# Performance work log

Hardware: AMD Instinct MI355X
Metric: run time of the kernel (lower is better)

The kernel has to match this reference:

```python
import jax, jax.numpy as jnp
import numpy as np

N = 100000   # nodes
E = 1600000  # edges (before self-loops)
H = 4        # heads
C = 16       # out channels per head
NEG_SLOPE = 0.2


def _gat_layer(x, src, dst, W, a_src, a_dst, b):
    # x: [N, Fin]; W: [Fin, H*C]; a_src/a_dst: [H, C]; b: [H*C]
    h = (x @ W).reshape(N, H, C)                       # [N, H, C]
    e_s = jnp.einsum('nhc,hc->nh', h, a_src)           # [N, H]
    e_d = jnp.einsum('nhc,hc->nh', h, a_dst)           # [N, H]
    e = e_s[src] + e_d[dst]                            # [E', H]
    e = jax.nn.leaky_relu(e, NEG_SLOPE)
    # segment softmax over destination nodes
    m = jax.ops.segment_max(e, dst, num_segments=N)    # [N, H]
    ex = jnp.exp(e - m[dst])
    s = jax.ops.segment_sum(ex, dst, num_segments=N)   # [N, H]
    alpha = ex / (s[dst] + 1e-16)                      # [E', H]
    msg = alpha[:, :, None] * h[src]                   # [E', H, C]
    out = jax.ops.segment_sum(msg, dst, num_segments=N)  # [N, H, C]
    return out.reshape(N, H * C) + b


def setup_inputs() -> dict:
    key = jax.random.key(0)
    ks = jax.random.split(key, 24)
    g = lambda k, shp, sc=0.1: (jax.random.normal(k, shp, jnp.float32) * sc)
    inp = {
        'x': jax.random.normal(ks[0], (N, 1), jnp.float32),
        'edge_index': jax.random.randint(ks[1], (2, E), 0, N, dtype=jnp.int32),
        # GAT layer 0: in=1
        'W0': g(ks[2], (1, H * C)), 'as0': g(ks[3], (H, C)), 'ad0': g(ks[4], (H, C)), 'b0': jnp.zeros((H * C,), jnp.float32),
        # GAT layer 1: in=64
        'W1': g(ks[5], (H * C, H * C)), 'as1': g(ks[6], (H, C)), 'ad1': g(ks[7], (H, C)), 'b1': jnp.zeros((H * C,), jnp.float32),
        # GAT layer 2: in=64
        'W2': g(ks[8], (H * C, H * C)), 'as2': g(ks[9], (H, C)), 'ad2': g(ks[10], (H, C)), 'b2': jnp.zeros((H * C,), jnp.float32),
        # latent MLP: Linear(64,64) -> ReLU -> Linear(64,16)
        'lw1': g(ks[11], (H * C, 64)), 'lb1': jnp.zeros((64,), jnp.float32),
        'lw2': g(ks[12], (64, 16)), 'lb2': jnp.zeros((16,), jnp.float32),
        # decoder: Linear(16,4) -> Softmax
        'dw': g(ks[13], (16, 4)), 'db': jnp.zeros((4,), jnp.float32),
    }
    return inp


def reference(x, edge_index, W0, as0, ad0, b0, W1, as1, ad1, b1, W2, as2, ad2, b2, lw1, lb1, lw2, lb2, dw, db):
    # add self-loops (PyG GATConv default add_self_loops=True)
    loops = jnp.arange(N, dtype=edge_index.dtype)
    src = jnp.concatenate([edge_index[0], loops])
    dst = jnp.concatenate([edge_index[1], loops])
    h = _gat_layer(x, src, dst, W0, as0, ad0, b0)
    h = _gat_layer(h, src, dst, W1, as1, ad1, b1)
    h = _gat_layer(h, src, dst, W2, as2, ad2, b2)
    h = jax.nn.relu(h @ lw1 + lb1)
    h = h @ lw2 + lb2
    logits = h @ dw + db
    return jax.nn.softmax(logits, axis=-1)
```

## Files before the change

kernel.cpp:

```cpp
#include <hip/hip_runtime.h>
#include <hip/hip_fp16.h>
#include <math.h>

#define NN 100000
#define EE 1600000
#define EP (EE + NN)
#define NEG 0.2f
#define TN 128
#define BW 256
#define NB 391
#define CHUNK 4096
#define SSTRIDE 5120
#define SCAP 5120

typedef __attribute__((ext_vector_type(2))) float floatx2;

__device__ inline unsigned pk_fp8x4(float a, float b, float c, float d) {
    unsigned r = __builtin_amdgcn_cvt_pk_fp8_f32(a, b, 0u, false);
    r = __builtin_amdgcn_cvt_pk_fp8_f32(c, d, r, true);
    return r;
}

__device__ __forceinline__ void accum_fp8p(uint2 raw, float p, floatx2* acc) {
    floatx2 p2; p2[0] = p; p2[1] = p;
    acc[0] += p2 * __builtin_amdgcn_cvt_pk_f32_fp8(raw.x, false);
    acc[1] += p2 * __builtin_amdgcn_cvt_pk_f32_fp8(raw.x, true);
    acc[2] += p2 * __builtin_amdgcn_cvt_pk_f32_fp8(raw.y, false);
    acc[3] += p2 * __builtin_amdgcn_cvt_pk_f32_fp8(raw.y, true);
}

__device__ __forceinline__ int wave_iscan(int v, int lane) {
#pragma unroll
    for (int o = 1; o < 64; o <<= 1) {
        int t = __shfl_up(v, o);
        if (lane >= o) v += t;
    }
    return v;
}


__global__ __launch_bounds__(512) void partition_k(const int* __restrict__ ei, int* __restrict__ gcur,
                                                   unsigned int* __restrict__ arena) {
    __shared__ int lh[512], lcur[512], lbase[512];
    __shared__ int wsum[8];
    __shared__ unsigned int staged[CHUNK];
    __shared__ unsigned short stb[CHUNK];
    int tid = threadIdx.x;
    int lane = tid & 63, wid = tid >> 6;
    int c0 = blockIdx.x * CHUNK;
    int csize = min(CHUNK, EP - c0);
    lh[tid] = 0;
    __syncthreads();
    unsigned int myv[8];
    int myb[8];
#pragma unroll
    for (int i = 0; i < 8; i++) {
        int e = c0 + i * 512 + tid;
        if (e < c0 + csize) {
            int d = (e < EE) ? ei[EE + e] : (e - EE);
            int sv = (e < EE) ? ei[e] : d;
            int b = d >> 8;
            myv[i] = ((unsigned)(d - (b << 8)) << 17) | (unsigned)sv;
            myb[i] = b;
            atomicAdd(&lh[b], 1);
        } else myb[i] = -1;
    }
    __syncthreads();
    int v = lh[tid];
    int isc = wave_iscan(v, lane);
    if (lane == 63) wsum[wid] = isc;
    __syncthreads();
    if (tid == 0) {
        int run = 0;
#pragma unroll
        for (int w = 0; w < 8; w++) { int t = wsum[w]; wsum[w] = run; run += t; }
    }
    __syncthreads();
    int excl = isc - v + wsum[wid];
    lcur[tid] = excl;
    __syncthreads();
#pragma unroll
    for (int i = 0; i < 8; i++) {
        if (myb[i] >= 0) {
            int idx = atomicAdd(&lcur[myb[i]], 1);
            staged[idx] = myv[i];
            stb[idx] = (unsigned short)myb[i];
        }
    }
    __syncthreads();
    if (tid < NB && v > 0) {
        int base = atomicAdd(&gcur[tid], v);
        lbase[tid] = tid * SSTRIDE + base - excl;
    }
    __syncthreads();
    for (int i = tid; i < csize; i += 512) {
        unsigned int val = staged[i];
        arena[lbase[stb[i]] + i] = val;
    }
}

__global__ __launch_bounds__(512) void bscan_k(const int* __restrict__ gcur, int* __restrict__ bbase,
                                               int* __restrict__ rowptr) {
    __shared__ int s[512];
    int tid = threadIdx.x;
    int v = (tid < NB) ? gcur[tid] : 0;
    s[tid] = v;
    __syncthreads();
    for (int o = 1; o < 512; o <<= 1) {
        int t = (tid >= o) ? s[tid - o] : 0;
        __syncthreads();
        s[tid] += t;
        __syncthreads();
    }
    int excl = s[tid] - v;
    if (tid <= NB) bbase[tid] = excl;
    if (tid == 0) rowptr[NN] = EP;
}

__global__ __launch_bounds__(512) void csr_scatter_k(const int* __restrict__ bbase, const int* __restrict__ gcur,
                                                     const unsigned int* __restrict__ arena,
                                                     int* __restrict__ rowptr, int* __restrict__ edge_src) {
    __shared__ int cnt[256], sc[256];
    __shared__ int wsum[4];
    __shared__ unsigned int stg[SCAP];
    int tid = threadIdx.x;
    int b = blockIdx.x;
    int e0 = bbase[b];
    int sz = gcur[b];
    int abase = b * SSTRIDE;
    if (tid < 256) cnt[tid] = 0;
    __syncthreads();
    for (int i = tid; i < sz; i += 512) {
        unsigned int v = arena[abase + i];
        if (i < SCAP) stg[i] = v;
        atomicAdd(&cnt[v >> 17], 1);
    }
    __syncthreads();
    if (tid < 256) {
        int lane = tid & 63, wid = tid >> 6;
        int v = cnt[tid];
        int isc = wave_iscan(v, lane);
        if (lane == 63) wsum[wid] = isc;
        __syncthreads();
        if (tid == 0) {
            int run = 0;
#pragma unroll
            for (int w = 0; w < 4; w++) { int t = wsum[w]; wsum[w] = run; run += t; }
        }
        __syncthreads();
        int excl = isc - v + wsum[wid];
        int d = (b << 8) + tid;
        if (d < NN) rowptr[d] = e0 + excl;
        sc[tid] = excl;
    } else {
        __syncthreads();
        __syncthreads();
    }
    __syncthreads();
    for (int i = tid; i < sz; i += 512) {
        unsigned int val = (i < SCAP) ? stg[i] : arena[abase + i];
        int dl = val >> 17;
        int p = atomicAdd(&sc[dl], 1);
        edge_src[e0 + p] = (int)(val & 0x1FFFFu);
    }
}


__global__ __launch_bounds__(256) void gather0_k(const float* __restrict__ x, const float* __restrict__ W0,
                                                 const float* __restrict__ as_, const float* __restrict__ ad_,
                                                 const int* __restrict__ rowptr, const int* __restrict__ edge_src,
                                                 const float* __restrict__ b, __half* __restrict__ hout) {
    __shared__ float W0l[64], asl[64], adl[64], bl[64];
    int tid = threadIdx.x;
    if (tid < 64) { W0l[tid] = W0[tid]; asl[tid] = as_[tid]; adl[tid] = ad_[tid]; bl[tid] = b[tid]; }
    __syncthreads();
    int wv = (blockIdx.x * 256 + tid) >> 6;
    int lane = tid & 63;
    if (wv >= NN) return;
    int q = lane >> 2, head = lane & 3;
    float cs = 0.f, cd = 0.f;
#pragma unroll
    for (int c = 0; c < 16; c++) {
        float w = W0l[head * 16 + c];
        cs += w * asl[head * 16 + c];
        cd += w * adl[head * 16 + c];
    }
    int beg = rowptr[wv], end = rowptr[wv + 1];
    float xd = x[wv];
    float num = 0.f, den = 0.f;
    for (int e0 = beg; e0 < end; e0 += 16) {
        int e = e0 + q;
        bool vld = e < end;
        int ee = vld ? e : (end - 1);
        int src = edge_src[ee];
        float xs = x[src];
        float ev = xs * cs + xd * cd;
        ev = ev > 0.f ? ev : NEG * ev;
        float p = vld ? __expf(ev) : 0.f;
        num += p * xs;
        den += p;
    }
    num += __shfl_xor(num, 4);  num += __shfl_xor(num, 8);
    num += __shfl_xor(num, 16); num += __shfl_xor(num, 32);
    den += __shfl_xor(den, 4);  den += __shfl_xor(den, 8);
    den += __shfl_xor(den, 16); den += __shfl_xor(den, 32);
    float nh = __shfl(num, lane >> 4);
    float dh = __shfl(den, lane >> 4);
    float val = nh / (dh + 1e-16f);
    float hv = val * W0l[lane] + bl[lane];
    hout[((size_t)wv << 6) + lane] = __float2half(hv);
}


__global__ __launch_bounds__(256) void transform64_k(const __half* __restrict__ hin, const float* __restrict__ W,
                                                     const float* __restrict__ as_, const float* __restrict__ ad_,
                                                     unsigned char* __restrict__ h8, float* __restrict__ es, float* __restrict__ ed) {
    __shared__ float At[64 * TN];
    __shared__ float Wl[64 * 64];
    int tid = threadIdx.x;
    for (int i = tid; i < 4096; i += 256) Wl[i] = W[i];
    int n0 = blockIdx.x * TN;
    {
        int row = tid >> 1, hf = tid & 1;
        int n = n0 + row;
        const uint4* src = (const uint4*)(hin + ((size_t)n << 6) + (hf << 5));
#pragma unroll
        for (int i = 0; i < 4; i++) {
            uint4 raw = make_uint4(0, 0, 0, 0);
            if (n < NN) raw = src[i];
            __half2* hh = (__half2*)&raw;
            int c = (hf << 5) + (i << 3);
#pragma unroll
            for (int j = 0; j < 4; j++) {
                float2 f = __half22float2(hh[j]);
                At[(c + 2 * j) * TN + row]     = f.x;
                At[(c + 2 * j + 1) * TN + row] = f.y;
            }
        }
    }
    __syncthreads();
    int c = tid & 15, r = tid >> 4;
    float acc[8][4];
#pragma unroll
    for (int i = 0; i < 8; i++)
#pragma unroll
        for (int j = 0; j < 4; j++) acc[i][j] = 0.f;
#pragma unroll 4
    for (int k = 0; k < 64; k++) {
        float4 a0 = *(float4*)&At[k * TN + r * 8];
        float4 a1 = *(float4*)&At[k * TN + r * 8 + 4];
        float4 w  = *(float4*)&Wl[k * 64 + c * 4];
        float av[8] = {a0.x, a0.y, a0.z, a0.w, a1.x, a1.y, a1.z, a1.w};
#pragma unroll
        for (int i = 0; i < 8; i++) {
            acc[i][0] += av[i] * w.x; acc[i][1] += av[i] * w.y;
            acc[i][2] += av[i] * w.z; acc[i][3] += av[i] * w.w;
        }
    }
    int head = c >> 2, qq = c & 3;
    float as0v = as_[head * 16 + qq * 4], as1v = as_[head * 16 + qq * 4 + 1];
    float as2v = as_[head * 16 + qq * 4 + 2], as3v = as_[head * 16 + qq * 4 + 3];
    float ad0v = ad_[head * 16 + qq * 4], ad1v = ad_[head * 16 + qq * 4 + 1];
    float ad2v = ad_[head * 16 + qq * 4 + 2], ad3v = ad_[head * 16 + qq * 4 + 3];
#pragma unroll
    for (int i = 0; i < 8; i++) {
        int n = n0 + r * 8 + i;
        float pes = acc[i][0] * as0v + acc[i][1] * as1v + acc[i][2] * as2v + acc[i][3] * as3v;
        float ped = acc[i][0] * ad0v + acc[i][1] * ad1v + acc[i][2] * ad2v + acc[i][3] * ad3v;
        pes += __shfl_xor(pes, 1); pes += __shfl_xor(pes, 2);
        ped += __shfl_xor(ped, 1); ped += __shfl_xor(ped, 2);
        if (n < NN) {
            unsigned rq = pk_fp8x4(acc[i][0], acc[i][1], acc[i][2], acc[i][3]);
            *(unsigned*)(h8 + ((size_t)n << 6) + (c << 2)) = rq;
            if (qq == 0) { es[n * 4 + head] = pes; ed[n * 4 + head] = ped; }
        }
    }
}


__global__ __launch_bounds__(256) void gather_k(const unsigned char* __restrict__ h8, const float* __restrict__ es,
                                                const float* __restrict__ ed, const int* __restrict__ rowptr,
                                                const int* __restrict__ edge_src, const float* __restrict__ b,
                                                __half* __restrict__ hout) {
    int pr = (blockIdx.x * 256 + threadIdx.x) >> 6;
    int lane = threadIdx.x & 63;
    int nA = pr * 2;
    if (nA >= NN) return;
    int nB = nA + 1;
    bool hasB = nB < NN;
    int q = lane >> 3, j = lane & 7, head = j >> 1;
    const unsigned char* h8j = h8 + (j << 3);
    int begA = rowptr[nA], endA = rowptr[nA + 1];
    int begB = hasB ? rowptr[nB] : begA, endB = hasB ? rowptr[nB + 1] : begA;
    float edvA = ed[nA * 4 + head];
    float edvB = hasB ? ed[nB * 4 + head] : 0.f;
    floatx2 accA[4], accB[4];
#pragma unroll
    for (int t = 0; t < 4; t++) { accA[t] = (floatx2)(0.f); accB[t] = (floatx2)(0.f); }
    float sA = 0.f, sB = 0.f;
    int iters = max((endA - begA + 7) >> 3, (endB - begB + 7) >> 3);
    for (int k = 0; k < iters; k++) {
        int eA = begA + (k << 3) + q;
        int eB = begB + (k << 3) + q;
        bool vA = eA < endA;
        bool vB = eB < endB;
        int srcA = edge_src[vA ? eA : begA];
        int srcB = edge_src[vB ? eB : begB];
        uint2 rawA = *(const uint2*)(h8j + ((unsigned)srcA << 6));
        float esvA = es[srcA * 4 + head];
        uint2 rawB = *(const uint2*)(h8j + ((unsigned)srcB << 6));
        float esvB = es[srcB * 4 + head];
        float evA = esvA + edvA; evA = evA > 0.f ? evA : NEG * evA;
        float evB = esvB + edvB; evB = evB > 0.f ? evB : NEG * evB;
        float pA = vA ? __expf(evA) : 0.f;
        float pB = vB ? __expf(evB) : 0.f;
        accum_fp8p(rawA, pA, accA);
        accum_fp8p(rawB, pB, accB);
        sA += pA;
        sB += pB;
    }
    float fA[8], fB[8];
#pragma unroll
    for (int t = 0; t < 4; t++) {
        fA[2 * t] = accA[t][0]; fA[2 * t + 1] = accA[t][1];
        fB[2 * t] = accB[t][0]; fB[2 * t + 1] = accB[t][1];
    }
#pragma unroll
    for (int t = 0; t < 8; t++) {
        fA[t] += __shfl_xor(fA[t], 8);
        fA[t] += __shfl_xor(fA[t], 16);
        fA[t] += __shfl_xor(fA[t], 32);
        fB[t] += __shfl_xor(fB[t], 8);
        fB[t] += __shfl_xor(fB[t], 16);
        fB[t] += __shfl_xor(fB[t], 32);
    }
    sA += __shfl_xor(sA, 8); sA += __shfl_xor(sA, 16); sA += __shfl_xor(sA, 32);
    sB += __shfl_xor(sB, 8); sB += __shfl_xor(sB, 16); sB += __shfl_xor(sB, 32);
    if (q == 0) {
        const float4* bp = (const float4*)(b + j * 8);
        float4 b0 = bp[0], b1 = bp[1];
        {
            float inv = 1.0f / (sA + 1e-16f);
            union { __half2 h2[4]; uint4 u; } pk;
            pk.h2[0] = __floats2half2_rn(fA[0] * inv + b0.x, fA[1] * inv + b0.y);
            pk.h2[1] = __floats2half2_rn(fA[2] * inv + b0.z, fA[3] * inv + b0.w);
            pk.h2[2] = __floats2half2_rn(fA[4] * inv + b1.x, fA[5] * inv + b1.y);
            pk.h2[3] = __floats2half2_rn(fA[6] * inv + b1.z, fA[7] * inv + b1.w);
            *(uint4*)(hout + ((size_t)nA << 6) + (j << 3)) = pk.u;
        }
        if (hasB) {
            float inv = 1.0f / (sB + 1e-16f);
            union { __half2 h2[4]; uint4 u; } pk;
            pk.h2[0] = __floats2half2_rn(fB[0] * inv + b0.x, fB[1] * inv + b0.y);
            pk.h2[1] = __floats2half2_rn(fB[2] * inv + b0.z, fB[3] * inv + b0.w);
            pk.h2[2] = __floats2half2_rn(fB[4] * inv + b1.x, fB[5] * inv + b1.y);
            pk.h2[3] = __floats2half2_rn(fB[6] * inv + b1.z, fB[7] * inv + b1.w);
            *(uint4*)(hout + ((size_t)nB << 6) + (j << 3)) = pk.u;
        }
    }
}


__global__ __launch_bounds__(256) void mlp_k(const __half* __restrict__ h, const float* __restrict__ lw1,
                                             const float* __restrict__ lb1, const float* __restrict__ lw2,
                                             const float* __restrict__ lb2, const float* __restrict__ dw,
                                             const float* __restrict__ db, float* __restrict__ out) {
    __shared__ float At[64 * TN];
    __shared__ float W1l[4096];
    __shared__ float W2l[1024];
    __shared__ float dwl[64];
    __shared__ float dbl[4];
    int tid = threadIdx.x;
    for (int i = tid; i < 4096; i += 256) W1l[i] = lw1[i];
    for (int i = tid; i < 1024; i += 256) W2l[i] = lw2[i];
    if (tid < 64) dwl[tid] = dw[tid];
    if (tid < 4) dbl[tid] = db[tid];
    int n0 = blockIdx.x * TN;
    {
        int row = tid >> 1, hf = tid & 1;
        int n = n0 + row;
        const uint4* src = (const uint4*)(h + ((size_t)n << 6) + (hf << 5));
#pragma unroll
        for (int i = 0; i < 4; i++) {
            uint4 raw = make_uint4(0, 0, 0, 0);
            if (n < NN) raw = src[i];
            __half2* hh = (__half2*)&raw;
            int c = (hf << 5) + (i << 3);
#pragma unroll
            for (int j = 0; j < 4; j++) {
                float2 f = __half22float2(hh[j]);
                At[(c + 2 * j) * TN + row]     = f.x;
                At[(c + 2 * j + 1) * TN + row] = f.y;
            }
        }
    }
    __syncthreads();
    int c = tid & 15, r = tid >> 4;
    float acc[8][4];
#pragma unroll
    for (int i = 0; i < 8; i++)
#pragma unroll
        for (int j = 0; j < 4; j++) acc[i][j] = 0.f;
#pragma unroll 4
    for (int k = 0; k < 64; k++) {
        float4 a0 = *(float4*)&At[k * TN + r * 8];
        float4 a1 = *(float4*)&At[k * TN + r * 8 + 4];
        float4 w  = *(float4*)&W1l[k * 64 + c * 4];
        float av[8] = {a0.x, a0.y, a0.z, a0.w, a1.x, a1.y, a1.z, a1.w};
#pragma unroll
        for (int i = 0; i < 8; i++) {
            acc[i][0] += av[i] * w.x; acc[i][1] += av[i] * w.y;
            acc[i][2] += av[i] * w.z; acc[i][3] += av[i] * w.w;
        }
    }
    float b1v0 = lb1[c * 4], b1v1 = lb1[c * 4 + 1], b1v2 = lb1[c * 4 + 2], b1v3 = lb1[c * 4 + 3];
    __syncthreads();
#pragma unroll
    for (int i = 0; i < 8; i++) {
        int n = r * 8 + i;
        At[(c * 4 + 0) * TN + n] = fmaxf(acc[i][0] + b1v0, 0.f);
        At[(c * 4 + 1) * TN + n] = fmaxf(acc[i][1] + b1v1, 0.f);
        At[(c * 4 + 2) * TN + n] = fmaxf(acc[i][2] + b1v2, 0.f);
        At[(c * 4 + 3) * TN + n] = fmaxf(acc[i][3] + b1v3, 0.f);
    }
    __syncthreads();
    float acc2[8];
#pragma unroll
    for (int i = 0; i < 8; i++) acc2[i] = 0.f;
#pragma unroll 4
    for (int k = 0; k < 64; k++) {
        float4 a0 = *(float4*)&At[k * TN + r * 8];
        float4 a1 = *(float4*)&At[k * TN + r * 8 + 4];
        float wv = W2l[k * 16 + c];
        acc2[0] += a0.x * wv; acc2[1] += a0.y * wv; acc2[2] += a0.z * wv; acc2[3] += a0.w * wv;
        acc2[4] += a1.x * wv; acc2[5] += a1.y * wv; acc2[6] += a1.z * wv; acc2[7] += a1.w * wv;
    }
    float b2v = lb2[c];
#pragma unroll
    for (int i = 0; i < 8; i++) W1l[c * TN + r * 8 + i] = acc2[i] + b2v;
    __syncthreads();
    if (tid < TN) {
        int n = n0 + tid;
        if (n < NN) {
            float lg0 = dbl[0], lg1 = dbl[1], lg2 = dbl[2], lg3 = dbl[3];
#pragma unroll
            for (int k = 0; k < 16; k++) {
                float a = W1l[k * TN + tid];
                lg0 += a * dwl[k * 4];     lg1 += a * dwl[k * 4 + 1];
                lg2 += a * dwl[k * 4 + 2]; lg3 += a * dwl[k * 4 + 3];
            }
            float mx = fmaxf(fmaxf(lg0, lg1), fmaxf(lg2, lg3));
            float e0 = __expf(lg0 - mx), e1 = __expf(lg1 - mx), e2 = __expf(lg2 - mx), e3 = __expf(lg3 - mx);
            float inv = 1.0f / (e0 + e1 + e2 + e3);
            *(float4*)(out + (size_t)n * 4) = make_float4(e0 * inv, e1 * inv, e2 * inv, e3 * inv);
        }
    }
}


extern "C" void kernel_launch(void* const* d_in, const int* in_sizes, int n_in,
                              void* d_out, int out_size, void* d_ws, size_t ws_size,
                              hipStream_t stream) {
    const float* x   = (const float*)d_in[0];
    const int*   ei  = (const int*)d_in[1];
    const float* W0  = (const float*)d_in[2];
    const float* as0 = (const float*)d_in[3];
    const float* ad0 = (const float*)d_in[4];
    const float* b0  = (const float*)d_in[5];
    const float* W1  = (const float*)d_in[6];
    const float* as1 = (const float*)d_in[7];
    const float* ad1 = (const float*)d_in[8];
    const float* b1  = (const float*)d_in[9];
    const float* W2  = (const float*)d_in[10];
    const float* as2 = (const float*)d_in[11];
    const float* ad2 = (const float*)d_in[12];
    const float* b2  = (const float*)d_in[13];
    const float* lw1 = (const float*)d_in[14];
    const float* lb1 = (const float*)d_in[15];
    const float* lw2 = (const float*)d_in[16];
    const float* lb2 = (const float*)d_in[17];
    const float* dw  = (const float*)d_in[18];
    const float* db  = (const float*)d_in[19];
    float* out = (float*)d_out;

    char* p = (char*)d_ws;
    size_t off = 0;
    auto alloc = [&](size_t n) -> void* {
        void* r = p + off;
        off = (off + n + 255) & ~(size_t)255;
        return r;
    };
    __half* hB     = (__half*)alloc((size_t)NN * 64 * 2);
    __half* hC     = (__half*)alloc((size_t)NN * 64 * 2);
    unsigned char* h8 = (unsigned char*)alloc((size_t)NN * 64);
    float*  es     = (float*)alloc((size_t)NN * 4 * 4);
    float*  ed     = (float*)alloc((size_t)NN * 4 * 4);
    int*    rowptr = (int*)alloc((size_t)(NN + 1) * 4);
    int*    edge_src = (int*)alloc((size_t)EP * 4);
    unsigned int* arena = (unsigned int*)alloc((size_t)NB * SSTRIDE * 4);
    int*    gcur   = (int*)alloc(512 * 4);
    int*    bbase  = (int*)alloc(513 * 4);

    hipMemsetAsync(gcur, 0, 512 * 4, stream);

    partition_k<<<(EP + CHUNK - 1) / CHUNK, 512, 0, stream>>>(ei, gcur, arena);
    bscan_k<<<1, 512, 0, stream>>>(gcur, bbase, rowptr);
    csr_scatter_k<<<NB, 512, 0, stream>>>(bbase, gcur, arena, rowptr, edge_src);

    int nb_tile = (NN + TN - 1) / TN;
    int nb_wave = (NN + 3) / 4;
    int nb_pair = ((NN + 1) / 2 + 3) / 4;

    gather0_k<<<nb_wave, 256, 0, stream>>>(x, W0, as0, ad0, rowptr, edge_src, b0, hB);

    transform64_k<<<nb_tile, 256, 0, stream>>>(hB, W1, as1, ad1, h8, es, ed);
    gather_k<<<nb_pair, 256, 0, stream>>>(h8, es, ed, rowptr, edge_src, b1, hC);

    transform64_k<<<nb_tile, 256, 0, stream>>>(hC, W2, as2, ad2, h8, es, ed);
    gather_k<<<nb_pair, 256, 0, stream>>>(h8, es, ed, rowptr, edge_src, b2, hB);

    mlp_k<<<nb_tile, 256, 0, stream>>>(hB, lw1, lb1, lw2, lb2, dw, db, out);
}
```

Baseline: 311.2 us.

## Fuse each GAT gather with the next transform or MLP through LDS tiles

Merges the per-layer gather kernel with the following 64x64 transform (and the last gather with the MLP/decoder) so each 128-node tile's aggregated features stay in swizzled fp16 LDS instead of going through global fp16 buffers. This cuts the launch count from six to three and removes the global write and read of the intermediate fp16 node features. Intermediate buffers are double-buffered (h8a/h8b, es/ed pairs) so a fused kernel can read the previous layer's output while writing its own. In exchange, each 512-thread block does the gather serially per wave (16 nodes per wave) before the GEMM, which could lower latency hiding and occupancy because of the larger LDS footprint.

```diff
diff --git a/kernel.cpp b/kernel.cpp
--- a/kernel.cpp
+++ b/kernel.cpp
@@ -7,7 +7,6 @@
 #define EP (EE + NN)
 #define NEG 0.2f
 #define TN 128
-#define BW 256
 #define NB 391
 #define CHUNK 4096
 #define SSTRIDE 5120
@@ -36,6 +35,145 @@
         if (lane >= o) v += t;
     }
     return v;
+}
+
+__device__ __forceinline__ int hoff(int nl, int slot) {
+    return (nl << 7) + (((slot ^ (nl >> 2)) & 7) << 4);
+}
+
+__device__ __forceinline__ void gemm64_lds(const unsigned short* hbuf, const float* Wl,
+                                           int c, int r, float acc[4][4]) {
+#pragma unroll
+    for (int i = 0; i < 4; i++)
+#pragma unroll
+        for (int j = 0; j < 4; j++) acc[i][j] = 0.f;
+    for (int kb = 0; kb < 8; kb++) {
+        float4 w[8];
+#pragma unroll
+        for (int kk = 0; kk < 8; kk++) w[kk] = *(const float4*)&Wl[(kb * 8 + kk) * 64 + c * 4];
+#pragma unroll
+        for (int i = 0; i < 4; i++) {
+            int nl = r * 4 + i;
+            uint4 a = *(const uint4*)((const char*)hbuf + hoff(nl, kb));
+            const __half2* hh = (const __half2*)&a;
+#pragma unroll
+            for (int kk = 0; kk < 4; kk++) {
+                float2 f = __half22float2(hh[kk]);
+                acc[i][0] += f.x * w[2 * kk].x + f.y * w[2 * kk + 1].x;
+                acc[i][1] += f.x * w[2 * kk].y + f.y * w[2 * kk + 1].y;
+                acc[i][2] += f.x * w[2 * kk].z + f.y * w[2 * kk + 1].z;
+                acc[i][3] += f.x * w[2 * kk].w + f.y * w[2 * kk + 1].w;
+            }
+        }
+    }
+}
+
+__device__ __forceinline__ void trans_epi(const float acc[4][4], const float* as_, const float* ad_,
+                                          unsigned char* h8o, float* eso, float* edo,
+                                          int n0, int c, int r) {
+    int head = c >> 2, qq = c & 3;
+    float as0v = as_[head * 16 + qq * 4], as1v = as_[head * 16 + qq * 4 + 1];
+    float as2v = as_[head * 16 + qq * 4 + 2], as3v = as_[head * 16 + qq * 4 + 3];
+    float ad0v = ad_[head * 16 + qq * 4], ad1v = ad_[head * 16 + qq * 4 + 1];
+    float ad2v = ad_[head * 16 + qq * 4 + 2], ad3v = ad_[head * 16 + qq * 4 + 3];
+#pragma unroll
+    for (int i = 0; i < 4; i++) {
+        int n = n0 + r * 4 + i;
+        float pes = acc[i][0] * as0v + acc[i][1] * as1v + acc[i][2] * as2v + acc[i][3] * as3v;
+        float ped = acc[i][0] * ad0v + acc[i][1] * ad1v + acc[i][2] * ad2v + acc[i][3] * ad3v;
+        pes += __shfl_xor(pes, 1); pes += __shfl_xor(pes, 2);
+        ped += __shfl_xor(ped, 1); ped += __shfl_xor(ped, 2);
+        if (n < NN) {
+            unsigned rq = pk_fp8x4(acc[i][0], acc[i][1], acc[i][2], acc[i][3]);
+            *(unsigned*)(h8o + ((size_t)n << 6) + (c << 2)) = rq;
+            if (qq == 0) { eso[n * 4 + head] = pes; edo[n * 4 + head] = ped; }
+        }
+    }
+}
+
+__device__ __forceinline__ void gather_rounds(const unsigned char* __restrict__ h8i,
+                                              const float* __restrict__ esi, const float* __restrict__ edi,
+                                              const int* __restrict__ rowptr, const int* __restrict__ edge_src,
+                                              const float* __restrict__ bg,
+                                              unsigned short* hbuf, int n0, int tid) {
+    int lane = tid & 63, wid = tid >> 6;
+    int q = lane >> 3, j = lane & 7, head = j >> 1;
+    const unsigned char* h8j = h8i + (j << 3);
+    const float4* bp = (const float4*)(bg + j * 8);
+    float4 bb0 = bp[0], bb1 = bp[1];
+    for (int rr = 0; rr < 8; rr++) {
+        int nlA = wid * 16 + rr * 2;
+        int nA = n0 + nlA;
+        if (nA >= NN) break;
+        int nB = nA + 1;
+        bool hasB = nB < NN;
+        int begA = rowptr[nA], endA = rowptr[nA + 1];
+        int begB = hasB ? rowptr[nB] : begA, endB = hasB ? rowptr[nB + 1] : begA;
+        float edvA = edi[nA * 4 + head];
+        float edvB = hasB ? edi[nB * 4 + head] : 0.f;
+        floatx2 accA[4], accB[4];
+#pragma unroll
+        for (int t = 0; t < 4; t++) { accA[t] = (floatx2)(0.f); accB[t] = (floatx2)(0.f); }
+        float sA = 0.f, sB = 0.f;
+        int iters = max((endA - begA + 7) >> 3, (endB - begB + 7) >> 3);
+        for (int k = 0; k < iters; k++) {
+            int eA = begA + (k << 3) + q;
+            int eB = begB + (k << 3) + q;
+            bool vA = eA < endA;
+            bool vB = eB < endB;
+            int srcA = edge_src[vA ? eA : begA];
+            int srcB = edge_src[vB ? eB : begB];
+            uint2 rawA = *(const uint2*)(h8j + ((unsigned)srcA << 6));
+            float esvA = esi[srcA * 4 + head];
+            uint2 rawB = *(const uint2*)(h8j + ((unsigned)srcB << 6));
+            float esvB = esi[srcB * 4 + head];
+            float evA = esvA + edvA; evA = evA > 0.f ? evA : NEG * evA;
+            float evB = esvB + edvB; evB = evB > 0.f ? evB : NEG * evB;
+            float pA = vA ? __expf(evA) : 0.f;
+            float pB = vB ? __expf(evB) : 0.f;
+            accum_fp8p(rawA, pA, accA);
+            accum_fp8p(rawB, pB, accB);
+            sA += pA;
+            sB += pB;
+        }
+        float fA[8], fB[8];
+#pragma unroll
+        for (int t = 0; t < 4; t++) {
+            fA[2 * t] = accA[t][0]; fA[2 * t + 1] = accA[t][1];
+            fB[2 * t] = accB[t][0]; fB[2 * t + 1] = accB[t][1];
+        }
+#pragma unroll
+        for (int t = 0; t < 8; t++) {
+            fA[t] += __shfl_xor(fA[t], 8);
+            fA[t] += __shfl_xor(fA[t], 16);
+            fA[t] += __shfl_xor(fA[t], 32);
+            fB[t] += __shfl_xor(fB[t], 8);
+            fB[t] += __shfl_xor(fB[t], 16);
+            fB[t] += __shfl_xor(fB[t], 32);
+        }
+        sA += __shfl_xor(sA, 8); sA += __shfl_xor(sA, 16); sA += __shfl_xor(sA, 32);
+        sB += __shfl_xor(sB, 8); sB += __shfl_xor(sB, 16); sB += __shfl_xor(sB, 32);
+        if (q == 0) {
+            {
+                float inv = 1.0f / (sA + 1e-16f);
+                union { __half2 h2[4]; uint4 u; } pk;
+                pk.h2[0] = __floats2half2_rn(fA[0] * inv + bb0.x, fA[1] * inv + bb0.y);
+                pk.h2[1] = __floats2half2_rn(fA[2] * inv + bb0.z, fA[3] * inv + bb0.w);
+                pk.h2[2] = __floats2half2_rn(fA[4] * inv + bb1.x, fA[5] * inv + bb1.y);
+                pk.h2[3] = __floats2half2_rn(fA[6] * inv + bb1.z, fA[7] * inv + bb1.w);
+                *(uint4*)((char*)hbuf + hoff(nlA, j)) = pk.u;
+            }
+            if (hasB) {
+                float inv = 1.0f / (sB + 1e-16f);
+                union { __half2 h2[4]; uint4 u; } pk;
+                pk.h2[0] = __floats2half2_rn(fB[0] * inv + bb0.x, fB[1] * inv + bb0.y);
+                pk.h2[1] = __floats2half2_rn(fB[2] * inv + bb0.z, fB[3] * inv + bb0.w);
+                pk.h2[2] = __floats2half2_rn(fB[4] * inv + bb1.x, fB[5] * inv + bb1.y);
+                pk.h2[3] = __floats2half2_rn(fB[6] * inv + bb1.z, fB[7] * inv + bb1.w);
+                *(uint4*)((char*)hbuf + hoff(nlA + 1, j)) = pk.u;
+            }
+        }
+    }
 }
 
 
@@ -166,278 +304,149 @@
 }
 
 
-__global__ __launch_bounds__(256) void gather0_k(const float* __restrict__ x, const float* __restrict__ W0,
-                                                 const float* __restrict__ as_, const float* __restrict__ ad_,
-                                                 const int* __restrict__ rowptr, const int* __restrict__ edge_src,
-                                                 const float* __restrict__ b, __half* __restrict__ hout) {
+__global__ __launch_bounds__(512) void g0t_k(const float* __restrict__ x, const float* __restrict__ W0,
+                                             const float* __restrict__ as0_, const float* __restrict__ ad0_,
+                                             const float* __restrict__ b0_,
+                                             const int* __restrict__ rowptr, const int* __restrict__ edge_src,
+                                             const float* __restrict__ W1, const float* __restrict__ as1_,
+                                             const float* __restrict__ ad1_,
+                                             unsigned char* __restrict__ h8o, float* __restrict__ eso,
+                                             float* __restrict__ edo) {
+    __shared__ __align__(16) unsigned short hbuf[TN * 64];
+    __shared__ float Wl[4096];
     __shared__ float W0l[64], asl[64], adl[64], bl[64];
     int tid = threadIdx.x;
-    if (tid < 64) { W0l[tid] = W0[tid]; asl[tid] = as_[tid]; adl[tid] = ad_[tid]; bl[tid] = b[tid]; }
-    __syncthreads();
-    int wv = (blockIdx.x * 256 + tid) >> 6;
-    int lane = tid & 63;
-    if (wv >= NN) return;
-    int q = lane >> 2, head = lane & 3;
+    for (int i = tid; i < 4096; i += 512) Wl[i] = W1[i];
+    if (tid < 64) { W0l[tid] = W0[tid]; asl[tid] = as0_[tid]; adl[tid] = ad0_[tid]; bl[tid] = b0_[tid]; }
+    __syncthreads();
+    int n0 = blockIdx.x * TN;
+    int lane = tid & 63, wid = tid >> 6;
+    int q4 = lane >> 2, head4 = lane & 3;
     float cs = 0.f, cd = 0.f;
 #pragma unroll
-    for (int c = 0; c < 16; c++) {
-        float w = W0l[head * 16 + c];
-        cs += w * asl[head * 16 + c];
-        cd += w * adl[head * 16 + c];
-    }
-    int beg = rowptr[wv], end = rowptr[wv + 1];
-    float xd = x[wv];
-    float num = 0.f, den = 0.f;
-    for (int e0 = beg; e0 < end; e0 += 16) {
-        int e = e0 + q;
-        bool vld = e < end;
-        int ee = vld ? e : (end - 1);
-        int src = edge_src[ee];
-        float xs = x[src];
-        float ev = xs * cs + xd * cd;
-        ev = ev > 0.f ? ev : NEG * ev;
-        float p = vld ? __expf(ev) : 0.f;
-        num += p * xs;
-        den += p;
-    }
-    num += __shfl_xor(num, 4);  num += __shfl_xor(num, 8);
-    num += __shfl_xor(num, 16); num += __shfl_xor(num, 32);
-    den += __shfl_xor(den, 4);  den += __shfl_xor(den, 8);
-    den += __shfl_xor(den, 16); den += __shfl_xor(den, 32);
-    float nh = __shfl(num, lane >> 4);
-    float dh = __shfl(den, lane >> 4);
-    float val = nh / (dh + 1e-16f);
-    float hv = val * W0l[lane] + bl[lane];
-    hout[((size_t)wv << 6) + lane] = __float2half(hv);
-}
-
-
-__global__ __launch_bounds__(256) void transform64_k(const __half* __restrict__ hin, const float* __restrict__ W,
-                                                     const float* __restrict__ as_, const float* __restrict__ ad_,
-                                                     unsigned char* __restrict__ h8, float* __restrict__ es, float* __restrict__ ed) {
-    __shared__ float At[64 * TN];
-    __shared__ float Wl[64 * 64];
+    for (int cc = 0; cc < 16; cc++) {
+        float w = W0l[head4 * 16 + cc];
+        cs += w * asl[head4 * 16 + cc];
+        cd += w * adl[head4 * 16 + cc];
+    }
+    for (int rr = 0; rr < 16; rr++) {
+        int nl = wid * 16 + rr;
+        int wv = n0 + nl;
+        if (wv >= NN) break;
+        int beg = rowptr[wv], end = rowptr[wv + 1];
+        float xd = x[wv];
+        float num = 0.f, den = 0.f;
+        for (int e0 = beg; e0 < end; e0 += 16) {
+            int e = e0 + q4;
+            bool vld = e < end;
+            int ee = vld ? e : (end - 1);
+            int src = edge_src[ee];
+            float xs = x[src];
+            float ev = xs * cs + xd * cd;
+            ev = ev > 0.f ? ev : NEG * ev;
+            float p = vld ? __expf(ev) : 0.f;
+            num += p * xs;
+            den += p;
+        }
+        num += __shfl_xor(num, 4);  num += __shfl_xor(num, 8);
+        num += __shfl_xor(num, 16); num += __shfl_xor(num, 32);
+        den += __shfl_xor(den, 4);  den += __shfl_xor(den, 8);
+        den += __shfl_xor(den, 16); den += __shfl_xor(den, 32);
+        float nh = __shfl(num, lane >> 4);
+        float dh = __shfl(den, lane >> 4);
+        float val = nh / (dh + 1e-16f);
+        float hv = val * W0l[lane] + bl[lane];
+        *(__half*)((char*)hbuf + hoff(nl, lane >> 3) + ((lane & 7) << 1)) = __float2half(hv);
+    }
+    __syncthreads();
+    int c = tid & 15, r = tid >> 4;
+    float acc[4][4];
+    gemm64_lds(hbuf, Wl, c, r, acc);
+    trans_epi(acc, as1_, ad1_, h8o, eso, edo, n0, c, r);
+}
+
+
+__global__ __launch_bounds__(512) void gt_k(const unsigned char* __restrict__ h8i, const float* __restrict__ esi,
+                                            const float* __restrict__ edi, const int* __restrict__ rowptr,
+                                            const int* __restrict__ edge_src, const float* __restrict__ bg,
+                                            const float* __restrict__ W, const float* __restrict__ as_,
+                                            const float* __restrict__ ad_,
+                                            unsigned char* __restrict__ h8o, float* __restrict__ eso,
+                                            float* __restrict__ edo) {
+    __shared__ __align__(16) unsigned short hbuf[TN * 64];
+    __shared__ float Wl[4096];
     int tid = threadIdx.x;
-    for (int i = tid; i < 4096; i += 256) Wl[i] = W[i];
+    for (int i = tid; i < 4096; i += 512) Wl[i] = W[i];
     int n0 = blockIdx.x * TN;
-    {
-        int row = tid >> 1, hf = tid & 1;
-        int n = n0 + row;
-        const uint4* src = (const uint4*)(hin + ((size_t)n << 6) + (hf << 5));
-#pragma unroll
-        for (int i = 0; i < 4; i++) {
-            uint4 raw = make_uint4(0, 0, 0, 0);
-            if (n < NN) raw = src[i];
-            __half2* hh = (__half2*)&raw;
-            int c = (hf << 5) + (i << 3);
-#pragma unroll
-            for (int j = 0; j < 4; j++) {
-                float2 f = __half22float2(hh[j]);
-                At[(c + 2 * j) * TN + row]     = f.x;
-                At[(c + 2 * j + 1) * TN + row] = f.y;
-            }
-        }
-    }
+    gather_rounds(h8i, esi, edi, rowptr, edge_src, bg, hbuf, n0, tid);
     __syncthreads();
     int c = tid & 15, r = tid >> 4;
-    float acc[8][4];
-#pragma unroll
-    for (int i = 0; i < 8; i++)
-#pragma unroll
-        for (int j = 0; j < 4; j++) acc[i][j] = 0.f;
-#pragma unroll 4
-    for (int k = 0; k < 64; k++) {
-        float4 a0 = *(float4*)&At[k * TN + r * 8];
-        float4 a1 = *(float4*)&At[k * TN + r * 8 + 4];
-        float4 w  = *(float4*)&Wl[k * 64 + c * 4];
-        float av[8] = {a0.x, a0.y, a0.z, a0.w, a1.x, a1.y, a1.z, a1.w};
-#pragma unroll
-        for (int i = 0; i < 8; i++) {
-            acc[i][0] += av[i] * w.x; acc[i][1] += av[i] * w.y;
-            acc[i][2] += av[i] * w.z; acc[i][3] += av[i] * w.w;
-        }
-    }
-    int head = c >> 2, qq = c & 3;
-    float as0v = as_[head * 16 + qq * 4], as1v = as_[head * 16 + qq * 4 + 1];
-    float as2v = as_[head * 16 + qq * 4 + 2], as3v = as_[head * 16 + qq * 4 + 3];
-    float ad0v = ad_[head * 16 + qq * 4], ad1v = ad_[head * 16 + qq * 4 + 1];
-    float ad2v = ad_[head * 16 + qq * 4 + 2], ad3v = ad_[head * 16 + qq * 4 + 3];
-#pragma unroll
-    for (int i = 0; i < 8; i++) {
-        int n = n0 + r * 8 + i;
-        float pes = acc[i][0] * as0v + acc[i][1] * as1v + acc[i][2] * as2v + acc[i][3] * as3v;
-        float ped = acc[i][0] * ad0v + acc[i][1] * ad1v + acc[i][2] * ad2v + acc[i][3] * ad3v;
-        pes += __shfl_xor(pes, 1); pes += __shfl_xor(pes, 2);
-        ped += __shfl_xor(ped, 1); ped += __shfl_xor(ped, 2);
-        if (n < NN) {
-            unsigned rq = pk_fp8x4(acc[i][0], acc[i][1], acc[i][2], acc[i][3]);
-            *(unsigned*)(h8 + ((size_t)n << 6) + (c << 2)) = rq;
-            if (qq == 0) { es[n * 4 + head] = pes; ed[n * 4 + head] = ped; }
-        }
-    }
-}
-
-
-__global__ __launch_bounds__(256) void gather_k(const unsigned char* __restrict__ h8, const float* __restrict__ es,
-                                                const float* __restrict__ ed, const int* __restrict__ rowptr,
-                                                const int* __restrict__ edge_src, const float* __restrict__ b,
-                                                __half* __restrict__ hout) {
-    int pr = (blockIdx.x * 256 + threadIdx.x) >> 6;
-    int lane = threadIdx.x & 63;
-    int nA = pr * 2;
-    if (nA >= NN) return;
-    int nB = nA + 1;
-    bool hasB = nB < NN;
-    int q = lane >> 3, j = lane & 7, head = j >> 1;
-    const unsigned char* h8j = h8 + (j << 3);
-    int begA = rowptr[nA], endA = rowptr[nA + 1];
-    int begB = hasB ? rowptr[nB] : begA, endB = hasB ? rowptr[nB + 1] : begA;
-    float edvA = ed[nA * 4 + head];
-    float edvB = hasB ? ed[nB * 4 + head] : 0.f;
-    floatx2 accA[4], accB[4];
-#pragma unroll
-    for (int t = 0; t < 4; t++) { accA[t] = (floatx2)(0.f); accB[t] = (floatx2)(0.f); }
-    float sA = 0.f, sB = 0.f;
-    int iters = max((endA - begA + 7) >> 3, (endB - begB + 7) >> 3);
-    for (int k = 0; k < iters; k++) {
-        int eA = begA + (k << 3) + q;
-        int eB = begB + (k << 3) + q;
-        bool vA = eA < endA;
-        bool vB = eB < endB;
-        int srcA = edge_src[vA ? eA : begA];
-        int srcB = edge_src[vB ? eB : begB];
-        uint2 rawA = *(const uint2*)(h8j + ((unsigned)srcA << 6));
-        float esvA = es[srcA * 4 + head];
-        uint2 rawB = *(const uint2*)(h8j + ((unsigned)srcB << 6));
-        float esvB = es[srcB * 4 + head];
-        float evA = esvA + edvA; evA = evA > 0.f ? evA : NEG * evA;
-        float evB = esvB + edvB; evB = evB > 0.f ? evB : NEG * evB;
-        float pA = vA ? __expf(evA) : 0.f;
-        float pB = vB ? __expf(evB) : 0.f;
-        accum_fp8p(rawA, pA, accA);
-        accum_fp8p(rawB, pB, accB);
-        sA += pA;
-        sB += pB;
-    }
-    float fA[8], fB[8];
-#pragma unroll
-    for (int t = 0; t < 4; t++) {
-        fA[2 * t] = accA[t][0]; fA[2 * t + 1] = accA[t][1];
-        fB[2 * t] = accB[t][0]; fB[2 * t + 1] = accB[t][1];
-    }
-#pragma unroll
-    for (int t = 0; t < 8; t++) {
-        fA[t] += __shfl_xor(fA[t], 8);
-        fA[t] += __shfl_xor(fA[t], 16);
-        fA[t] += __shfl_xor(fA[t], 32);
-        fB[t] += __shfl_xor(fB[t], 8);
-        fB[t] += __shfl_xor(fB[t], 16);
-        fB[t] += __shfl_xor(fB[t], 32);
-    }
-    sA += __shfl_xor(sA, 8); sA += __shfl_xor(sA, 16); sA += __shfl_xor(sA, 32);
-    sB += __shfl_xor(sB, 8); sB += __shfl_xor(sB, 16); sB += __shfl_xor(sB, 32);
-    if (q == 0) {
-        const float4* bp = (const float4*)(b + j * 8);
-        float4 b0 = bp[0], b1 = bp[1];
-        {
-            float inv = 1.0f / (sA + 1e-16f);
-            union { __half2 h2[4]; uint4 u; } pk;
-            pk.h2[0] = __floats2half2_rn(fA[0] * inv + b0.x, fA[1] * inv + b0.y);
-            pk.h2[1] = __floats2half2_rn(fA[2] * inv + b0.z, fA[3] * inv + b0.w);
-            pk.h2[2] = __floats2half2_rn(fA[4] * inv + b1.x, fA[5] * inv + b1.y);
-            pk.h2[3] = __floats2half2_rn(fA[6] * inv + b1.z, fA[7] * inv + b1.w);
-            *(uint4*)(hout + ((size_t)nA << 6) + (j << 3)) = pk.u;
-        }
-        if (hasB) {
-            float inv = 1.0f / (sB + 1e-16f);
-            union { __half2 h2[4]; uint4 u; } pk;
-            pk.h2[0] = __floats2half2_rn(fB[0] * inv + b0.x, fB[1] * inv + b0.y);
-            pk.h2[1] = __floats2half2_rn(fB[2] * inv + b0.z, fB[3] * inv + b0.w);
-            pk.h2[2] = __floats2half2_rn(fB[4] * inv + b1.x, fB[5] * inv + b1.y);
-            pk.h2[3] = __floats2half2_rn(fB[6] * inv + b1.z, fB[7] * inv + b1.w);
-            *(uint4*)(hout + ((size_t)nB << 6) + (j << 3)) = pk.u;
-        }
-    }
-}
-
-
-__global__ __launch_bounds__(256) void mlp_k(const __half* __restrict__ h, const float* __restrict__ lw1,
-                                             const float* __restrict__ lb1, const float* __restrict__ lw2,
-                                             const float* __restrict__ lb2, const float* __restrict__ dw,
-                                             const float* __restrict__ db, float* __restrict__ out) {
-    __shared__ float At[64 * TN];
+    float acc[4][4];
+    gemm64_lds(hbuf, Wl, c, r, acc);
+    trans_epi(acc, as_, ad_, h8o, eso, edo, n0, c, r);
+}
+
+
+__global__ __launch_bounds__(512) void gm_k(const unsigned char* __restrict__ h8i, const float* __restrict__ esi,
+                                            const float* __restrict__ edi, const int* __restrict__ rowptr,
+                                            const int* __restrict__ edge_src, const float* __restrict__ bg,
+                                            const float* __restrict__ lw1, const float* __restrict__ lb1,
+                                            const float* __restrict__ lw2, const float* __restrict__ lb2,
+                                            const float* __restrict__ dw, const float* __restrict__ db,
+                                            float* __restrict__ out) {
+    __shared__ __align__(16) unsigned short hbuf[TN * 64];
     __shared__ float W1l[4096];
     __shared__ float W2l[1024];
-    __shared__ float dwl[64];
-    __shared__ float dbl[4];
+    __shared__ float a2t[16 * 132];
+    __shared__ float lb1l[64], lb2l[16], dwl[64], dbl[4];
     int tid = threadIdx.x;
-    for (int i = tid; i < 4096; i += 256) W1l[i] = lw1[i];
-    for (int i = tid; i < 1024; i += 256) W2l[i] = lw2[i];
-    if (tid < 64) dwl[tid] = dw[tid];
+    for (int i = tid; i < 4096; i += 512) W1l[i] = lw1[i];
+    for (int i = tid; i < 1024; i += 512) W2l[i] = lw2[i];
+    if (tid < 64) { lb1l[tid] = lb1[tid]; dwl[tid] = dw[tid]; }
+    if (tid < 16) lb2l[tid] = lb2[tid];
     if (tid < 4) dbl[tid] = db[tid];
     int n0 = blockIdx.x * TN;
-    {
-        int row = tid >> 1, hf = tid & 1;
-        int n = n0 + row;
-        const uint4* src = (const uint4*)(h + ((size_t)n << 6) + (hf << 5));
+    gather_rounds(h8i, esi, edi, rowptr, edge_src, bg, hbuf, n0, tid);
+    __syncthreads();
+    int c = tid & 15, r = tid >> 4;
+    float acc[4][4];
+    gemm64_lds(hbuf, W1l, c, r, acc);
+#pragma unroll
+    for (int i = 0; i < 4; i++) {
+        acc[i][0] = fmaxf(acc[i][0] + lb1l[c * 4 + 0], 0.f);
+        acc[i][1] = fmaxf(acc[i][1] + lb1l[c * 4 + 1], 0.f);
+        acc[i][2] = fmaxf(acc[i][2] + lb1l[c * 4 + 2], 0.f);
+        acc[i][3] = fmaxf(acc[i][3] + lb1l[c * 4 + 3], 0.f);
+    }
+    __syncthreads();
+#pragma unroll
+    for (int i = 0; i < 4; i++) {
+        int nl = r * 4 + i;
+        union { __half2 h2[2]; uint2 u; } pk;
+        pk.h2[0] = __floats2half2_rn(acc[i][0], acc[i][1]);
+        pk.h2[1] = __floats2half2_rn(acc[i][2], acc[i][3]);
+        *(uint2*)((char*)hbuf + hoff(nl, c >> 1) + ((c & 1) << 3)) = pk.u;
+    }
+    __syncthreads();
+    float acc2[4] = {0.f, 0.f, 0.f, 0.f};
+    for (int kb = 0; kb < 8; kb++) {
+        float w2v[8];
+#pragma unroll
+        for (int kk = 0; kk < 8; kk++) w2v[kk] = W2l[(kb * 8 + kk) * 16 + c];
 #pragma unroll
         for (int i = 0; i < 4; i++) {
-            uint4 raw = make_uint4(0, 0, 0, 0);
-            if (n < NN) raw = src[i];
-            __half2* hh = (__half2*)&raw;
-            int c = (hf << 5) + (i << 3);
-#pragma unroll
-            for (int j = 0; j < 4; j++) {
-                float2 f = __half22float2(hh[j]);
-                At[(c + 2 * j) * TN + row]     = f.x;
-                At[(c + 2 * j + 1) * TN + row] = f.y;
+            uint4 a = *(const uint4*)((const char*)hbuf + hoff(r * 4 + i, kb));
+            const __half2* hh = (const __half2*)&a;
+#pragma unroll
+            for (int kk = 0; kk < 4; kk++) {
+                float2 f = __half22float2(hh[kk]);
+                acc2[i] += f.x * w2v[2 * kk] + f.y * w2v[2 * kk + 1];
             }
         }
     }
-    __syncthreads();
-    int c = tid & 15, r = tid >> 4;
-    float acc[8][4];
-#pragma unroll
-    for (int i = 0; i < 8; i++)
-#pragma unroll
-        for (int j = 0; j < 4; j++) acc[i][j] = 0.f;
-#pragma unroll 4
-    for (int k = 0; k < 64; k++) {
-        float4 a0 = *(float4*)&At[k * TN + r * 8];
-        float4 a1 = *(float4*)&At[k * TN + r * 8 + 4];
-        float4 w  = *(float4*)&W1l[k * 64 + c * 4];
-        float av[8] = {a0.x, a0.y, a0.z, a0.w, a1.x, a1.y, a1.z, a1.w};
-#pragma unroll
-        for (int i = 0; i < 8; i++) {
-            acc[i][0] += av[i] * w.x; acc[i][1] += av[i] * w.y;
-            acc[i][2] += av[i] * w.z; acc[i][3] += av[i] * w.w;
-        }
-    }
-    float b1v0 = lb1[c * 4], b1v1 = lb1[c * 4 + 1], b1v2 = lb1[c * 4 + 2], b1v3 = lb1[c * 4 + 3];
-    __syncthreads();
-#pragma unroll
-    for (int i = 0; i < 8; i++) {
-        int n = r * 8 + i;
-        At[(c * 4 + 0) * TN + n] = fmaxf(acc[i][0] + b1v0, 0.f);
-        At[(c * 4 + 1) * TN + n] = fmaxf(acc[i][1] + b1v1, 0.f);
-        At[(c * 4 + 2) * TN + n] = fmaxf(acc[i][2] + b1v2, 0.f);
-        At[(c * 4 + 3) * TN + n] = fmaxf(acc[i][3] + b1v3, 0.f);
-    }
-    __syncthreads();
-    float acc2[8];
-#pragma unroll
-    for (int i = 0; i < 8; i++) acc2[i] = 0.f;
-#pragma unroll 4
-    for (int k = 0; k < 64; k++) {
-        float4 a0 = *(float4*)&At[k * TN + r * 8];
-        float4 a1 = *(float4*)&At[k * TN + r * 8 + 4];
-        float wv = W2l[k * 16 + c];
-        acc2[0] += a0.x * wv; acc2[1] += a0.y * wv; acc2[2] += a0.z * wv; acc2[3] += a0.w * wv;
-        acc2[4] += a1.x * wv; acc2[5] += a1.y * wv; acc2[6] += a1.z * wv; acc2[7] += a1.w * wv;
-    }
-    float b2v = lb2[c];
-#pragma unroll
-    for (int i = 0; i < 8; i++) W1l[c * TN + r * 8 + i] = acc2[i] + b2v;
+    float b2v = lb2l[c];
+#pragma unroll
+    for (int i = 0; i < 4; i++) a2t[c * 132 + r * 4 + i] = acc2[i] + b2v;
     __syncthreads();
     if (tid < TN) {
         int n = n0 + tid;
@@ -445,7 +454,7 @@
             float lg0 = dbl[0], lg1 = dbl[1], lg2 = dbl[2], lg3 = dbl[3];
 #pragma unroll
             for (int k = 0; k < 16; k++) {
-                float a = W1l[k * TN + tid];
+                float a = a2t[k * 132 + tid];
                 lg0 += a * dwl[k * 4];     lg1 += a * dwl[k * 4 + 1];
                 lg2 += a * dwl[k * 4 + 2]; lg3 += a * dwl[k * 4 + 3];
             }
@@ -490,11 +499,12 @@
         off = (off + n + 255) & ~(size_t)255;
         return r;
     };
-    __half* hB     = (__half*)alloc((size_t)NN * 64 * 2);
-    __half* hC     = (__half*)alloc((size_t)NN * 64 * 2);
-    unsigned char* h8 = (unsigned char*)alloc((size_t)NN * 64);
-    float*  es     = (float*)alloc((size_t)NN * 4 * 4);
-    float*  ed     = (float*)alloc((size_t)NN * 4 * 4);
+    unsigned char* h8a = (unsigned char*)alloc((size_t)NN * 64);
+    unsigned char* h8b = (unsigned char*)alloc((size_t)NN * 64);
+    float*  esa    = (float*)alloc((size_t)NN * 4 * 4);
+    float*  eda    = (float*)alloc((size_t)NN * 4 * 4);
+    float*  esb    = (float*)alloc((size_t)NN * 4 * 4);
+    float*  edb    = (float*)alloc((size_t)NN * 4 * 4);
     int*    rowptr = (int*)alloc((size_t)(NN + 1) * 4);
     int*    edge_src = (int*)alloc((size_t)EP * 4);
     unsigned int* arena = (unsigned int*)alloc((size_t)NB * SSTRIDE * 4);
@@ -507,17 +517,9 @@
     bscan_k<<<1, 512, 0, stream>>>(gcur, bbase, rowptr);
     csr_scatter_k<<<NB, 512, 0, stream>>>(bbase, gcur, arena, rowptr, edge_src);
 
-    int nb_tile = (NN + TN - 1) / TN;
-    int nb_wave = (NN + 3) / 4;
-    int nb_pair = ((NN + 1) / 2 + 3) / 4;
-
-    gather0_k<<<nb_wave, 256, 0, stream>>>(x, W0, as0, ad0, rowptr, edge_src, b0, hB);
-
-    transform64_k<<<nb_tile, 256, 0, stream>>>(hB, W1, as1, ad1, h8, es, ed);
-    gather_k<<<nb_pair, 256, 0, stream>>>(h8, es, ed, rowptr, edge_src, b1, hC);
-
-    transform64_k<<<nb_tile, 256, 0, stream>>>(hC, W2, as2, ad2, h8, es, ed);
-    gather_k<<<nb_pair, 256, 0, stream>>>(h8, es, ed, rowptr, edge_src, b2, hB);
-
-    mlp_k<<<nb_tile, 256, 0, stream>>>(hB, lw1, lb1, lw2, lb2, dw, db, out);
-}
+    int nb = (NN + TN - 1) / TN;
+
+    g0t_k<<<nb, 512, 0, stream>>>(x, W0, as0, ad0, b0, rowptr, edge_src, W1, as1, ad1, h8a, esa, eda);
+    gt_k<<<nb, 512, 0, stream>>>(h8a, esa, eda, rowptr, edge_src, b1, W2, as2, ad2, h8b, esb, edb);
+    gm_k<<<nb, 512, 0, stream>>>(h8b, esb, edb, rowptr, edge_src, b2, lw1, lb1, lw2, lb2, dw, db, out);
+}
```

New measurement: 423.5 us. 1.36x slower.

## Split fp8 feature table by head halves and gather in two passes

Applied to the files above, without the earlier changes.

The transform kernel now writes the fp8 node features as two separate 32-byte-per-node tables, one for heads 0-1 and one for heads 2-3. The gather kernel takes a pass index and runs once per half, accumulating only two heads. The aim is a smaller randomly-gathered working set that fits cache better. In exchange, edge indices, rowptr and attention scores are re-read in each pass, and the number of gather launches doubles.

```diff
diff --git a/kernel.cpp b/kernel.cpp
--- a/kernel.cpp
+++ b/kernel.cpp
@@ -19,14 +19,6 @@
     unsigned r = __builtin_amdgcn_cvt_pk_fp8_f32(a, b, 0u, false);
     r = __builtin_amdgcn_cvt_pk_fp8_f32(c, d, r, true);
     return r;
-}
-
-__device__ __forceinline__ void accum_fp8p(uint2 raw, float p, floatx2* acc) {
-    floatx2 p2; p2[0] = p; p2[1] = p;
-    acc[0] += p2 * __builtin_amdgcn_cvt_pk_f32_fp8(raw.x, false);
-    acc[1] += p2 * __builtin_amdgcn_cvt_pk_f32_fp8(raw.x, true);
-    acc[2] += p2 * __builtin_amdgcn_cvt_pk_f32_fp8(raw.y, false);
-    acc[3] += p2 * __builtin_amdgcn_cvt_pk_f32_fp8(raw.y, true);
 }
 
 __device__ __forceinline__ int wave_iscan(int v, int lane) {
@@ -262,6 +254,8 @@
     float as2v = as_[head * 16 + qq * 4 + 2], as3v = as_[head * 16 + qq * 4 + 3];
     float ad0v = ad_[head * 16 + qq * 4], ad1v = ad_[head * 16 + qq * 4 + 1];
     float ad2v = ad_[head * 16 + qq * 4 + 2], ad3v = ad_[head * 16 + qq * 4 + 3];
+    unsigned char* tb = (c < 8) ? h8 : (h8 + (size_t)NN * 32);
+    int co = (c & 7) << 2;
 #pragma unroll
     for (int i = 0; i < 8; i++) {
         int n = n0 + r * 8 + i;
@@ -271,7 +265,7 @@
         ped += __shfl_xor(ped, 1); ped += __shfl_xor(ped, 2);
         if (n < NN) {
             unsigned rq = pk_fp8x4(acc[i][0], acc[i][1], acc[i][2], acc[i][3]);
-            *(unsigned*)(h8 + ((size_t)n << 6) + (c << 2)) = rq;
+            *(unsigned*)(tb + ((size_t)n << 5) + co) = rq;
             if (qq == 0) { es[n * 4 + head] = pes; ed[n * 4 + head] = ped; }
         }
     }
@@ -281,22 +275,23 @@
 __global__ __launch_bounds__(256) void gather_k(const unsigned char* __restrict__ h8, const float* __restrict__ es,
                                                 const float* __restrict__ ed, const int* __restrict__ rowptr,
                                                 const int* __restrict__ edge_src, const float* __restrict__ b,
-                                                __half* __restrict__ hout) {
+                                                __half* __restrict__ hout, int pass) {
     int pr = (blockIdx.x * 256 + threadIdx.x) >> 6;
     int lane = threadIdx.x & 63;
     int nA = pr * 2;
     if (nA >= NN) return;
     int nB = nA + 1;
     bool hasB = nB < NN;
-    int q = lane >> 3, j = lane & 7, head = j >> 1;
-    const unsigned char* h8j = h8 + (j << 3);
+    int q = lane >> 3, j = lane & 7;
+    int head = (pass << 1) + (j >> 2);
+    const unsigned char* h8p = h8 + ((size_t)pass * NN * 32) + (j << 2);
     int begA = rowptr[nA], endA = rowptr[nA + 1];
     int begB = hasB ? rowptr[nB] : begA, endB = hasB ? rowptr[nB + 1] : begA;
     float edvA = ed[nA * 4 + head];
     float edvB = hasB ? ed[nB * 4 + head] : 0.f;
-    floatx2 accA[4], accB[4];
-#pragma unroll
-    for (int t = 0; t < 4; t++) { accA[t] = (floatx2)(0.f); accB[t] = (floatx2)(0.f); }
+    floatx2 accA[2], accB[2];
+    accA[0] = (floatx2)(0.f); accA[1] = (floatx2)(0.f);
+    accB[0] = (floatx2)(0.f); accB[1] = (floatx2)(0.f);
     float sA = 0.f, sB = 0.f;
     int iters = max((endA - begA + 7) >> 3, (endB - begB + 7) >> 3);
     for (int k = 0; k < iters; k++) {
@@ -306,27 +301,27 @@
         bool vB = eB < endB;
         int srcA = edge_src[vA ? eA : begA];
         int srcB = edge_src[vB ? eB : begB];
-        uint2 rawA = *(const uint2*)(h8j + ((unsigned)srcA << 6));
+        unsigned rawA = *(const unsigned*)(h8p + ((unsigned)srcA << 5));
         float esvA = es[srcA * 4 + head];
-        uint2 rawB = *(const uint2*)(h8j + ((unsigned)srcB << 6));
+        unsigned rawB = *(const unsigned*)(h8p + ((unsigned)srcB << 5));
         float esvB = es[srcB * 4 + head];
         float evA = esvA + edvA; evA = evA > 0.f ? evA : NEG * evA;
         float evB = esvB + edvB; evB = evB > 0.f ? evB : NEG * evB;
         float pA = vA ? __expf(evA) : 0.f;
         float pB = vB ? __expf(evB) : 0.f;
-        accum_fp8p(rawA, pA, accA);
-        accum_fp8p(rawB, pB, accB);
+        floatx2 p2A; p2A[0] = pA; p2A[1] = pA;
+        floatx2 p2B; p2B[0] = pB; p2B[1] = pB;
+        accA[0] += p2A * __builtin_amdgcn_cvt_pk_f32_fp8(rawA, false);
+        accA[1] += p2A * __builtin_amdgcn_cvt_pk_f32_fp8(rawA, true);
+        accB[0] += p2B * __builtin_amdgcn_cvt_pk_f32_fp8(rawB, false);
+        accB[1] += p2B * __builtin_amdgcn_cvt_pk_f32_fp8(rawB, true);
         sA += pA;
         sB += pB;
     }
-    float fA[8], fB[8];
+    float fA[4] = {accA[0][0], accA[0][1], accA[1][0], accA[1][1]};
+    float fB[4] = {accB[0][0], accB[0][1], accB[1][0], accB[1][1]};
 #pragma unroll
     for (int t = 0; t < 4; t++) {
-        fA[2 * t] = accA[t][0]; fA[2 * t + 1] = accA[t][1];
-        fB[2 * t] = accB[t][0]; fB[2 * t + 1] = accB[t][1];
-    }
-#pragma unroll
-    for (int t = 0; t < 8; t++) {
         fA[t] += __shfl_xor(fA[t], 8);
         fA[t] += __shfl_xor(fA[t], 16);
         fA[t] += __shfl_xor(fA[t], 32);
@@ -337,25 +332,20 @@
     sA += __shfl_xor(sA, 8); sA += __shfl_xor(sA, 16); sA += __shfl_xor(sA, 32);
     sB += __shfl_xor(sB, 8); sB += __shfl_xor(sB, 16); sB += __shfl_xor(sB, 32);
     if (q == 0) {
-        const float4* bp = (const float4*)(b + j * 8);
-        float4 b0 = bp[0], b1 = bp[1];
+        float4 bv = *(const float4*)(b + (pass << 5) + (j << 2));
         {
             float inv = 1.0f / (sA + 1e-16f);
-            union { __half2 h2[4]; uint4 u; } pk;
-            pk.h2[0] = __floats2half2_rn(fA[0] * inv + b0.x, fA[1] * inv + b0.y);
-            pk.h2[1] = __floats2half2_rn(fA[2] * inv + b0.z, fA[3] * inv + b0.w);
-            pk.h2[2] = __floats2half2_rn(fA[4] * inv + b1.x, fA[5] * inv + b1.y);
-            pk.h2[3] = __floats2half2_rn(fA[6] * inv + b1.z, fA[7] * inv + b1.w);
-            *(uint4*)(hout + ((size_t)nA << 6) + (j << 3)) = pk.u;
+            union { __half2 h2[2]; uint2 u; } pk;
+            pk.h2[0] = __floats2half2_rn(fA[0] * inv + bv.x, fA[1] * inv + bv.y);
+            pk.h2[1] = __floats2half2_rn(fA[2] * inv + bv.z, fA[3] * inv + bv.w);
+            *(uint2*)(hout + ((size_t)nA << 6) + (pass << 5) + (j << 2)) = pk.u;
         }
         if (hasB) {
             float inv = 1.0f / (sB + 1e-16f);
-            union { __half2 h2[4]; uint4 u; } pk;
-            pk.h2[0] = __floats2half2_rn(fB[0] * inv + b0.x, fB[1] * inv + b0.y);
-            pk.h2[1] = __floats2half2_rn(fB[2] * inv + b0.z, fB[3] * inv + b0.w);
-            pk.h2[2] = __floats2half2_rn(fB[4] * inv + b1.x, fB[5] * inv + b1.y);
-            pk.h2[3] = __floats2half2_rn(fB[6] * inv + b1.z, fB[7] * inv + b1.w);
-            *(uint4*)(hout + ((size_t)nB << 6) + (j << 3)) = pk.u;
+            union { __half2 h2[2]; uint2 u; } pk;
+            pk.h2[0] = __floats2half2_rn(fB[0] * inv + bv.x, fB[1] * inv + bv.y);
+            pk.h2[1] = __floats2half2_rn(fB[2] * inv + bv.z, fB[3] * inv + bv.w);
+            *(uint2*)(hout + ((size_t)nB << 6) + (pass << 5) + (j << 2)) = pk.u;
         }
     }
 }
@@ -514,10 +504,12 @@
     gather0_k<<<nb_wave, 256, 0, stream>>>(x, W0, as0, ad0, rowptr, edge_src, b0, hB);
 
     transform64_k<<<nb_tile, 256, 0, stream>>>(hB, W1, as1, ad1, h8, es, ed);
-    gather_k<<<nb_pair, 256, 0, stream>>>(h8, es, ed, rowptr, edge_src, b1, hC);
+    gather_k<<<nb_pair, 256, 0, stream>>>(h8, es, ed, rowptr, edge_src, b1, hC, 0);
+    gather_k<<<nb_pair, 256, 0, stream>>>(h8, es, ed, rowptr, edge_src, b1, hC, 1);
 
     transform64_k<<<nb_tile, 256, 0, stream>>>(hC, W2, as2, ad2, h8, es, ed);
-    gather_k<<<nb_pair, 256, 0, stream>>>(h8, es, ed, rowptr, edge_src, b2, hB);
+    gather_k<<<nb_pair, 256, 0, stream>>>(h8, es, ed, rowptr, edge_src, b2, hB, 0);
+    gather_k<<<nb_pair, 256, 0, stream>>>(h8, es, ed, rowptr, edge_src, b2, hB, 1);
 
     mlp_k<<<nb_tile, 256, 0, stream>>>(hB, lw1, lb1, lw2, lb2, dw, db, out);
 }
```

Result: slower. 358.7 us (+15.3%).
